# Kernel optimization log

Hardware: AMD Instinct MI355X
Metric: run time of the kernel (lower is better)

## Reference

```python
import jax, jax.numpy as jnp
import numpy as np

NHEAD = 4
DIM = 256

def rotate_half(x):
    # interleaved: out[..., ::2] = -x[..., 1::2]; out[..., 1::2] = x[..., ::2]
    xe = x[..., ::2]
    xo = x[..., 1::2]
    return jnp.stack([-xo, xe], axis=-1).reshape(x.shape)

def rope_2d(q, k, H, W):
    Dh = q.shape[-1]
    half = Dh // 2
    inv_freq = 1.0 / (10000.0 ** (jnp.arange(half, dtype=jnp.float32) / half))  # [half]
    yy, xx = jnp.meshgrid(jnp.arange(H, dtype=jnp.float32), jnp.arange(W, dtype=jnp.float32), indexing='ij')
    ang_y = yy.reshape(-1)[:, None] * inv_freq  # [N, half]
    ang_x = xx.reshape(-1)[:, None] * inv_freq  # [N, half]
    cy, sy = jnp.cos(ang_y), jnp.sin(ang_y)
    cx, sx = jnp.cos(ang_x), jnp.sin(ang_x)
    def rot(t):
        t1 = t[..., :half]          # y-rotated half
        t2 = t[..., half:2 * half]  # x-rotated half
        ty = t1 * cy + rotate_half(t1) * sy
        tx = t2 * cx + rotate_half(t2) * sx
        return jnp.concatenate([ty, tx, t[..., 2 * half:]], axis=-1)
    return rot(q), rot(k)

def layernorm(x, g, b, eps=1e-5):
    mu = jnp.mean(x, axis=-1, keepdims=True)
    var = jnp.var(x, axis=-1, keepdims=True)
    return (x - mu) / jnp.sqrt(var + eps) * g + b

def setup_inputs() -> dict:
    key = jax.random.key(0)
    ks = jax.random.split(key, 8)
    B, Hs, Ws, C = 4, 48, 48, DIM
    N = Hs * Ws
    s = 0.02
    return {
        'x': jax.random.normal(ks[0], (B, N, C), dtype=jnp.float32),
        'Wqkv': jax.random.normal(ks[1], (3 * C, C), dtype=jnp.float32) * s,
        'Wproj': jax.random.normal(ks[2], (C, C), dtype=jnp.float32) * s,
        'g1': jnp.ones((C,), jnp.float32), 'b1': jnp.zeros((C,), jnp.float32),
        'g2': jnp.ones((C,), jnp.float32), 'b2': jnp.zeros((C,), jnp.float32),
        'W1': jax.random.normal(ks[3], (4 * C, C), dtype=jnp.float32) * s,
        'bf1': jnp.zeros((4 * C,), jnp.float32),
        'W2': jax.random.normal(ks[4], (C, 4 * C), dtype=jnp.float32) * s,
        'bf2': jnp.zeros((C,), jnp.float32),
        'H': Hs, 'W': Ws,
    }

def reference(x, Wqkv, Wproj, g1, b1, g2, b2, W1, bf1, W2, bf2, H, W):
    B, N, C = x.shape
    dh = C // NHEAD
    qkv = (x @ Wqkv.T).reshape(B, N, 3, NHEAD, dh).transpose(2, 0, 3, 1, 4)  # [3,B,h,N,dh]
    q, k, v = qkv[0], qkv[1], qkv[2]
    q, k = rope_2d(q, k, H, W)
    scores = jnp.einsum('bhnd,bhmd->bhnm', q, k) / jnp.sqrt(jnp.float32(dh))
    attn = jax.nn.softmax(scores, axis=-1)  # drop_attn is identity (p=0)
    out = jnp.einsum('bhnm,bhmd->bhnd', attn, v).transpose(0, 2, 1, 3).reshape(B, N, C)
    x = x + out @ Wproj.T
    x = layernorm(x, g1, b1)
    h = jax.nn.gelu(x @ W1.T + bf1, approximate=False)
    x = x + h @ W2.T + bf2
    return layernorm(x, g2, b2)
```

## Files before the change

### kernel.cpp

```cpp
#include <hip/hip_runtime.h>
#include <hip/hip_bf16.h>
#include <math.h>

typedef __hip_bfloat16 bf16;
typedef __attribute__((ext_vector_type(8))) short short8;
typedef __attribute__((ext_vector_type(4))) short short4v;
typedef __attribute__((ext_vector_type(4))) float f32x4;
typedef __attribute__((ext_vector_type(4))) unsigned int u32x4;

#define NSEQ 2304
#define CDIM 256
#define NHD  4
#define DH   64

#if __has_builtin(__builtin_amdgcn_exp2f)
#define EXP2F __builtin_amdgcn_exp2f
#else
#define EXP2F exp2f
#endif

static __device__ __forceinline__ f32x4 mfma_bf16(short8 a, short8 b, f32x4 c) {
  return __builtin_amdgcn_mfma_f32_16x16x32_bf16(a, b, c, 0, 0, 0);
}
static __device__ __forceinline__ short8 ld8(const bf16* p) {
  return *reinterpret_cast<const short8*>(p);
}
static __device__ __forceinline__ short8 lds8(const bf16* p) {
  return *reinterpret_cast<const short8*>(p);
}
static __device__ __forceinline__ float b2f(short v) {
  unsigned int u = ((unsigned int)(unsigned short)v) << 16;
  return __uint_as_float(u);
}
static __device__ __forceinline__ short f2b(float f) {
  bf16 h = __float2bfloat16(f);
  return *reinterpret_cast<short*>(&h);
}
static __device__ __forceinline__ int swzb(int row, int off) {
  return (row << 7) + (off ^ ((row & 7) << 4));
}

__global__ __launch_bounds__(256) void detect_kernel(const void* __restrict__ xraw,
                                                     int* __restrict__ flag) {
  int t = threadIdx.x;
  const unsigned short* s = (const unsigned short*)xraw;
  int bad = 0;
#pragma unroll
  for (int i = 0; i < 8; ++i) {
    unsigned idx = (((unsigned)(t * 8 + i)) * 9173u) & ((1u << 20) - 1);
    unsigned short v = s[idx * 2];
    unsigned e = (v >> 7) & 0xFFu;
    if (e > 133u) bad++;
  }
  __shared__ int tot;
  if (t == 0) tot = 0;
  __syncthreads();
  atomicAdd(&tot, bad);
  __syncthreads();
  if (t == 0) flag[0] = (tot >= 16) ? 1 : 0;
}

__global__ __launch_bounds__(256) void cvt_all_kernel(const void* sx, const void* sqkv, const void* sproj,
                                                      const void* sw1, const void* sw2,
                                                      const void* g1, const void* b1, const void* g2,
                                                      const void* b2, const void* bias1, const void* bias2,
                                                      bf16* dx, bf16* dqkv, bf16* dproj,
                                                      bf16* dw1, bf16* dw2, bf16* dsm,
                                                      const int* __restrict__ flag) {
  int is32 = flag[0];
  int bid = blockIdx.x;
  const void* src; bf16* dst; int i4;
  if (bid < 2304)      { src = sx;    dst = dx;    i4 = bid * 256 + threadIdx.x; }
  else if (bid < 2496) { src = sqkv;  dst = dqkv;  i4 = (bid - 2304) * 256 + threadIdx.x; }
  else if (bid < 2560) { src = sproj; dst = dproj; i4 = (bid - 2496) * 256 + threadIdx.x; }
  else if (bid < 2816) { src = sw1;   dst = dw1;   i4 = (bid - 2560) * 256 + threadIdx.x; }
  else if (bid < 3072) { src = sw2;   dst = dw2;   i4 = (bid - 2816) * 256 + threadIdx.x; }
  else {
    const void* srcs[6] = {g1, b1, g2, b2, bias1, bias2};
    const int ns[6] = {256, 256, 256, 256, 1024, 256};
    const int off[6] = {0, 256, 512, 768, 1024, 2048};
    int t = threadIdx.x;
#pragma unroll
    for (int j = 0; j < 6; ++j)
      for (int i = t; i < ns[j]; i += 256) {
        if (is32) dsm[off[j] + i] = __float2bfloat16(((const float*)srcs[j])[i]);
        else      dsm[off[j] + i] = ((const bf16*)srcs[j])[i];
      }
    return;
  }
  if (is32) {
    float4 v = ((const float4*)src)[i4];
    short4v o;
    o[0] = f2b(v.x); o[1] = f2b(v.y); o[2] = f2b(v.z); o[3] = f2b(v.w);
    ((short4v*)dst)[i4] = o;
  } else {
    ((short4v*)dst)[i4] = ((const short4v*)src)[i4];
  }
}

__global__ __launch_bounds__(256, 1) void qkv_kernel(const bf16* __restrict__ X,
                                                     const bf16* __restrict__ Wqkv,
                                                     bf16* __restrict__ Q, bf16* __restrict__ K,
                                                     bf16* __restrict__ Vt,
                                                     const int* __restrict__ Wp) {
  int wave = threadIdx.x >> 6, lane = threadIdx.x & 63;
  int l15 = lane & 15, quad = lane >> 4;
  int m0 = (blockIdx.x * 4 + wave) * 64;
  int n0 = blockIdx.y * 64;
  const bf16* arow = X + (size_t)(m0 + l15) * CDIM + quad * 8;
  const bf16* brow = Wqkv + (size_t)(n0 + l15) * CDIM + quad * 8;
  f32x4 z = {0.f, 0.f, 0.f, 0.f};
  f32x4 acc[4][4];
#pragma unroll
  for (int j = 0; j < 4; ++j)
#pragma unroll
    for (int i = 0; i < 4; ++i) acc[j][i] = z;

  short8 a[4], b[4];
#pragma unroll
  for (int i = 0; i < 4; ++i) a[i] = ld8(arow + (size_t)i * 16 * CDIM);
#pragma unroll
  for (int j = 0; j < 4; ++j) b[j] = ld8(brow + (size_t)j * 16 * CDIM);
#pragma unroll
  for (int kk = 32; kk <= CDIM; kk += 32) {
    short8 an[4], bn[4];
    if (kk < CDIM) {
#pragma unroll
      for (int i = 0; i < 4; ++i) an[i] = ld8(arow + (size_t)i * 16 * CDIM + kk);
#pragma unroll
      for (int j = 0; j < 4; ++j) bn[j] = ld8(brow + (size_t)j * 16 * CDIM + kk);
    }
#pragma unroll
    for (int j = 0; j < 4; ++j)
#pragma unroll
      for (int i = 0; i < 4; ++i) acc[j][i] = mfma_bf16(b[j], a[i], acc[j][i]);
    if (kk < CDIM) {
#pragma unroll
      for (int i = 0; i < 4; ++i) a[i] = an[i];
#pragma unroll
      for (int j = 0; j < 4; ++j) b[j] = bn[j];
    }
  }

  int which = n0 >> 8, h = (n0 & 255) >> 6;
  if (which == 2) {
#pragma unroll
    for (int j = 0; j < 4; ++j) {
      int d0 = j * 16 + quad * 4;
#pragma unroll
      for (int i = 0; i < 4; ++i) {
        int gm = m0 + i * 16 + l15;
        int bb = gm / NSEQ, n = gm % NSEQ;
        int bh = bb * NHD + h;
#pragma unroll
        for (int r = 0; r < 4; ++r)
          Vt[((size_t)bh * DH + d0 + r) * NSEQ + n] = __float2bfloat16(acc[j][i][r]);
      }
    }
  } else {
    int Wv = Wp[0];
    if (Wv <= 0 || Wv > 65536) Wv = 48;
    bf16* dst = (which == 0) ? Q : K;
    const float cc = -0.28782313662425574f;
    const float EC1 = 0.7498942434f, EC2 = 0.5623413252f, EC3 = 0.4216965034f;
#pragma unroll
    for (int i = 0; i < 4; ++i) {
      int gm = m0 + i * 16 + l15;
      int bb = gm / NSEQ, n = gm % NSEQ;
      int bh = bb * NHD + h;
      int py = n / Wv, px = n - py * Wv;
#pragma unroll
      for (int j = 0; j < 4; ++j) {
        int d0 = j * 16 + quad * 4;
        float pos = (d0 & 32) ? (float)px : (float)py;
        int base = d0 & 31;
        float fb = __expf(cc * (float)base);
        float f0 = fb, f1 = fb * EC1, f2 = fb * EC2, f3 = fb * EC3;
        float s0, c0, s1, c1, s2, c2, s3, c3;
        __sincosf(pos * f0, &s0, &c0);
        __sincosf(pos * f1, &s1, &c1);
        __sincosf(pos * f2, &s2, &c2);
        __sincosf(pos * f3, &s3, &c3);
        float a0 = acc[j][i][0], a1 = acc[j][i][1], a2 = acc[j][i][2], a3 = acc[j][i][3];
        short4v ov;
        ov[0] = f2b(a0 * c0 - a1 * s0);
        ov[1] = f2b(a1 * c1 + a0 * s1);
        ov[2] = f2b(a2 * c2 - a3 * s2);
        ov[3] = f2b(a3 * c3 + a2 * s3);
        *reinterpret_cast<short4v*>(dst + ((size_t)bh * NSEQ + n) * DH + d0) = ov;
      }
    }
  }
}

__global__ __launch_bounds__(256, 4) void attn_kernel(const bf16* __restrict__ Q, const bf16* __restrict__ K,
                                                      const bf16* __restrict__ Vt, bf16* __restrict__ AO) {
  int bh = blockIdx.x, qt = blockIdx.y;
  int tid = threadIdx.x;
  int wave = tid >> 6, lane = tid & 63;
  int l15 = lane & 15, quad = lane >> 4;
  int qf = wave & 1;
  int ks = wave >> 1;
  int m0 = qt * 64 + qf * 32;
  const bf16* Qb = Q + (size_t)bh * NSEQ * DH;
  const bf16* Kb = K + (size_t)bh * NSEQ * DH;
  const bf16* Vb = Vt + (size_t)bh * DH * NSEQ;

  __shared__ __align__(16) char smem[32768];

  int r1 = tid >> 3, c1b = (tid & 7) * 16;
  int r1b = r1 + 32;

  const float QS = 0.18033688011112042f;
  short8 qa0 = ld8(Qb + (size_t)(m0 + l15) * DH + quad * 8);
  short8 qa1 = ld8(Qb + (size_t)(m0 + l15) * DH + 32 + quad * 8);
  short8 qb0 = ld8(Qb + (size_t)(m0 + 16 + l15) * DH + quad * 8);
  short8 qb1 = ld8(Qb + (size_t)(m0 + 16 + l15) * DH + 32 + quad * 8);
#pragma unroll
  for (int i = 0; i < 8; ++i) {
    qa0[i] = f2b(b2f(qa0[i]) * QS);
    qa1[i] = f2b(b2f(qa1[i]) * QS);
    qb0[i] = f2b(b2f(qb0[i]) * QS);
    qb1[i] = f2b(b2f(qb1[i]) * QS);
  }

  f32x4 z = {0.f, 0.f, 0.f, 0.f};
  f32x4 o[4] = {z, z, z, z};
  f32x4 o2[4] = {z, z, z, z};
  float l_run = 0.f, l_run2 = 0.f;

  *reinterpret_cast<short8*>(smem + swzb(r1, c1b))          = ld8(Kb + (size_t)r1 * DH + c1b / 2);
  *reinterpret_cast<short8*>(smem + swzb(r1b, c1b))         = ld8(Kb + (size_t)r1b * DH + c1b / 2);
  *reinterpret_cast<short8*>(smem + 16384 + swzb(r1, c1b))  = ld8(Vb + (size_t)r1 * NSEQ + c1b / 2);
  *reinterpret_cast<short8*>(smem + 16384 + swzb(r1b, c1b)) = ld8(Vb + (size_t)r1b * NSEQ + c1b / 2);
  __syncthreads();

  for (int it = 0; it < NSEQ / 64; ++it) {
    int cur = it & 1;
    bool more = (it + 1 < NSEQ / 64);

    short8 kpA, kpB, vpA, vpB;
    if (more) {
      int kn = (it + 1) * 64;
      kpA = ld8(Kb + (size_t)(kn + r1) * DH + c1b / 2);
      kpB = ld8(Kb + (size_t)(kn + r1b) * DH + c1b / 2);
      vpA = ld8(Vb + (size_t)r1 * NSEQ + kn + c1b / 2);
      vpB = ld8(Vb + (size_t)r1b * NSEQ + kn + c1b / 2);
    }

    const char* kb = smem + cur * 8192;
    const char* vb = smem + 16384 + cur * 8192;

    f32x4 s[2], s2[2];
#pragma unroll
    for (int kt = 0; kt < 2; ++kt) {
      int krow = ks * 32 + kt * 16 + l15;
      short8 kf0 = *reinterpret_cast<const short8*>(kb + swzb(krow, quad * 16));
      short8 kf1 = *reinterpret_cast<const short8*>(kb + swzb(krow, quad * 16 + 64));
      s[kt] = mfma_bf16(kf0, qa0, z);
      s[kt] = mfma_bf16(kf1, qa1, s[kt]);
      s2[kt] = mfma_bf16(kf0, qb0, z);
      s2[kt] = mfma_bf16(kf1, qb1, s2[kt]);
    }

    unsigned int A0, B0, A1, B1, C0, D0, C1, D1;
    {
      float p00 = EXP2F(s[0][0]), p01 = EXP2F(s[0][1]), p02 = EXP2F(s[0][2]), p03 = EXP2F(s[0][3]);
      float p10 = EXP2F(s[1][0]), p11 = EXP2F(s[1][1]), p12 = EXP2F(s[1][2]), p13 = EXP2F(s[1][3]);
      l_run += ((p00 + p01) + (p02 + p03)) + ((p10 + p11) + (p12 + p13));
      asm("v_cvt_pk_bf16_f32 %0, %1, %2" : "=v"(A0) : "v"(p00), "v"(p01));
      asm("v_cvt_pk_bf16_f32 %0, %1, %2" : "=v"(B0) : "v"(p02), "v"(p03));
      asm("v_cvt_pk_bf16_f32 %0, %1, %2" : "=v"(A1) : "v"(p10), "v"(p11));
      asm("v_cvt_pk_bf16_f32 %0, %1, %2" : "=v"(B1) : "v"(p12), "v"(p13));
      float q00 = EXP2F(s2[0][0]), q01 = EXP2F(s2[0][1]), q02 = EXP2F(s2[0][2]), q03 = EXP2F(s2[0][3]);
      float q10 = EXP2F(s2[1][0]), q11 = EXP2F(s2[1][1]), q12 = EXP2F(s2[1][2]), q13 = EXP2F(s2[1][3]);
      l_run2 += ((q00 + q01) + (q02 + q03)) + ((q10 + q11) + (q12 + q13));
      asm("v_cvt_pk_bf16_f32 %0, %1, %2" : "=v"(C0) : "v"(q00), "v"(q01));
      asm("v_cvt_pk_bf16_f32 %0, %1, %2" : "=v"(D0) : "v"(q02), "v"(q03));
      asm("v_cvt_pk_bf16_f32 %0, %1, %2" : "=v"(C1) : "v"(q10), "v"(q11));
      asm("v_cvt_pk_bf16_f32 %0, %1, %2" : "=v"(D1) : "v"(q12), "v"(q13));
    }
    asm("v_permlane32_swap_b32 %0, %1" : "+v"(A0), "+v"(A1));
    asm("v_permlane16_swap_b32 %0, %1" : "+v"(A0), "+v"(A1));
    asm("v_permlane32_swap_b32 %0, %1" : "+v"(B0), "+v"(B1));
    asm("v_permlane16_swap_b32 %0, %1" : "+v"(B0), "+v"(B1));
    asm("v_permlane32_swap_b32 %0, %1" : "+v"(C0), "+v"(C1));
    asm("v_permlane16_swap_b32 %0, %1" : "+v"(C0), "+v"(C1));
    asm("v_permlane32_swap_b32 %0, %1" : "+v"(D0), "+v"(D1));
    asm("v_permlane16_swap_b32 %0, %1" : "+v"(D0), "+v"(D1));

    u32x4 wA; wA[0] = A0; wA[1] = B0; wA[2] = A1; wA[3] = B1;
    u32x4 wB; wB[0] = C0; wB[1] = D0; wB[2] = C1; wB[3] = D1;
    short8 pfA = *reinterpret_cast<short8*>(&wA);
    short8 pfB = *reinterpret_cast<short8*>(&wB);

#pragma unroll
    for (int t = 0; t < 4; ++t) {
      short8 vf = *reinterpret_cast<const short8*>(vb + swzb(t * 16 + l15, ks * 64 + quad * 16));
      o[t] = mfma_bf16(vf, pfA, o[t]);
      o2[t] = mfma_bf16(vf, pfB, o2[t]);
    }

    if (more) {
      char* kn_ = smem + (1 - cur) * 8192;
      char* vn_ = smem + 16384 + (1 - cur) * 8192;
      *reinterpret_cast<short8*>(kn_ + swzb(r1, c1b))  = kpA;
      *reinterpret_cast<short8*>(kn_ + swzb(r1b, c1b)) = kpB;
      *reinterpret_cast<short8*>(vn_ + swzb(r1, c1b))  = vpA;
      *reinterpret_cast<short8*>(vn_ + swzb(r1b, c1b)) = vpB;
    }
    __syncthreads();
  }

  float* scr = (float*)smem;
  int slot = qf * 64 + lane;
  if (ks == 1) {
    float* p = scr + slot * 36;
#pragma unroll
    for (int t = 0; t < 4; ++t) {
      *reinterpret_cast<f32x4*>(p + t * 4) = o[t];
      *reinterpret_cast<f32x4*>(p + 16 + t * 4) = o2[t];
    }
    p[32] = l_run;
    p[33] = l_run2;
  }
  __syncthreads();
  if (ks == 0) {
    float* p = scr + slot * 36;
#pragma unroll
    for (int t = 0; t < 4; ++t) {
      f32x4 pa = *reinterpret_cast<f32x4*>(p + t * 4);
      f32x4 pb2 = *reinterpret_cast<f32x4*>(p + 16 + t * 4);
#pragma unroll
      for (int r = 0; r < 4; ++r) {
        o[t][r] += pa[r];
        o2[t][r] += pb2[r];
      }
    }
    l_run += p[32];
    l_run2 += p[33];

    l_run += __shfl_xor(l_run, 16);
    l_run += __shfl_xor(l_run, 32);
    l_run2 += __shfl_xor(l_run2, 16);
    l_run2 += __shfl_xor(l_run2, 32);
    float inv = 1.f / l_run;
    float inv2 = 1.f / l_run2;
    int b = bh >> 2, h = bh & 3;
    bf16* orow = AO + ((size_t)b * NSEQ + (m0 + l15)) * CDIM + h * DH;
    bf16* orow2 = AO + ((size_t)b * NSEQ + (m0 + 16 + l15)) * CDIM + h * DH;
#pragma unroll
    for (int t = 0; t < 4; ++t) {
      short4v ov, ov2;
#pragma unroll
      for (int r = 0; r < 4; ++r) {
        ov[r] = f2b(o[t][r] * inv);
        ov2[r] = f2b(o2[t][r] * inv2);
      }
      *reinterpret_cast<short4v*>(orow + t * 16 + quad * 4) = ov;
      *reinterpret_cast<short4v*>(orow2 + t * 16 + quad * 4) = ov2;
    }
  }
}

template <int KD, int EPI, int TI>
__global__ __launch_bounds__(256) void gemm128(const bf16* __restrict__ A, const bf16* __restrict__ Wm,
                                               const bf16* __restrict__ bias, const bf16* __restrict__ res,
                                               bf16* __restrict__ outp, int NC) {
  constexpr int KS = KD / 32;
  constexpr int AR = TI * 32;
  int tid = threadIdx.x;
  int wave = tid >> 6, lane = tid & 63;
  int l15 = lane & 15, quad = lane >> 4;
  int wm = (wave >> 1) * (TI * 16);
  int wn = (wave & 1) * 64;
  int m0 = blockIdx.x * AR;
  int n0 = blockIdx.y * 128;

  __shared__ __align__(16) bf16 abuf[2][AR * 40];
  __shared__ __align__(16) bf16 bbuf[2][128 * 40];

  int sr = tid >> 2, sc = (tid & 3) * 8;

  const bf16* ag[TI / 2];
#pragma unroll
  for (int u = 0; u < TI / 2; ++u) ag[u] = A + (size_t)(m0 + sr + u * 64) * KD + sc;
  const bf16* bg0 = Wm + (size_t)(n0 + sr) * KD + sc;
  const bf16* bg1 = Wm + (size_t)(n0 + 64 + sr) * KD + sc;

  f32x4 z = {0.f, 0.f, 0.f, 0.f};
  f32x4 acc[4][TI];
#pragma unroll
  for (int j = 0; j < 4; ++j)
#pragma unroll
    for (int i = 0; i < TI; ++i) acc[j][i] = z;

#pragma unroll
  for (int u = 0; u < TI / 2; ++u)
    *reinterpret_cast<short8*>(abuf[0] + (sr + u * 64) * 40 + sc) = ld8(ag[u]);
  *reinterpret_cast<short8*>(bbuf[0] + sr * 40 + sc) = ld8(bg0);
  *reinterpret_cast<short8*>(bbuf[0] + (64 + sr) * 40 + sc) = ld8(bg1);
  __syncthreads();

  for (int s = 0; s < KS; ++s) {
    int cur = s & 1;
    bool more = (s + 1 < KS);
    short8 anx[TI / 2], bnx0, bnx1;
    if (more) {
#pragma unroll
      for (int u = 0; u < TI / 2; ++u) anx[u] = ld8(ag[u] + (s + 1) * 32);
      bnx0 = ld8(bg0 + (s + 1) * 32);
      bnx1 = ld8(bg1 + (s + 1) * 32);
    }
    short8 af[TI], bf_[4];
#pragma unroll
    for (int i = 0; i < TI; ++i)
      af[i] = lds8(abuf[cur] + (size_t)(wm + i * 16 + l15) * 40 + quad * 8);
#pragma unroll
    for (int j = 0; j < 4; ++j)
      bf_[j] = lds8(bbuf[cur] + (size_t)(wn + j * 16 + l15) * 40 + quad * 8);
#pragma unroll
    for (int j = 0; j < 4; ++j)
#pragma unroll
      for (int i = 0; i < TI; ++i)
        acc[j][i] = mfma_bf16(bf_[j], af[i], acc[j][i]);
    if (more) {
#pragma unroll
      for (int u = 0; u < TI / 2; ++u)
        *reinterpret_cast<short8*>(abuf[1 - cur] + (sr + u * 64) * 40 + sc) = anx[u];
      *reinterpret_cast<short8*>(bbuf[1 - cur] + sr * 40 + sc) = bnx0;
      *reinterpret_cast<short8*>(bbuf[1 - cur] + (64 + sr) * 40 + sc) = bnx1;
    }
    __syncthreads();
  }

#pragma unroll
  for (int j = 0; j < 4; ++j) {
    int col0 = n0 + wn + j * 16 + quad * 4;
    float bb4[4];
    if (EPI != 0) {
      short4v bl = *reinterpret_cast<const short4v*>(bias + col0);
#pragma unroll
      for (int r = 0; r < 4; ++r) bb4[r] = b2f(bl[r]);
    }
#pragma unroll
    for (int i = 0; i < TI; ++i) {
      size_t idx = (size_t)(m0 + wm + i * 16 + l15) * NC + col0;
      short4v ov;
      if (EPI == 0) {
        short4v rl = *reinterpret_cast<const short4v*>(res + idx);
#pragma unroll
        for (int r = 0; r < 4; ++r) ov[r] = f2b(acc[j][i][r] + b2f(rl[r]));
      } else if (EPI == 1) {
#pragma unroll
        for (int r = 0; r < 4; ++r) {
          float hv = acc[j][i][r] + bb4[r];
          ov[r] = f2b(0.5f * hv * (1.f + erff(hv * 0.70710678118f)));
        }
      } else {
        short4v rl = *reinterpret_cast<const short4v*>(res + idx);
#pragma unroll
        for (int r = 0; r < 4; ++r) ov[r] = f2b(acc[j][i][r] + bb4[r] + b2f(rl[r]));
      }
      *reinterpret_cast<short4v*>(outp + idx) = ov;
    }
  }
}

template <int KD, int HASBIAS, int FINAL>
__global__ __launch_bounds__(256) void gemm_ln(const bf16* __restrict__ A, const bf16* __restrict__ Wm,
                                               const bf16* __restrict__ bias, const bf16* __restrict__ res,
                                               const bf16* __restrict__ g, const bf16* __restrict__ bv,
                                               void* __restrict__ outp, const int* __restrict__ flag) {
  constexpr int KS = KD / 32;
  int tid = threadIdx.x;
  int wave = tid >> 6, lane = tid & 63;
  int l15 = lane & 15, quad = lane >> 4;
  int wn = wave * 64;
  int m0 = blockIdx.x * 32;
  int is32 = FINAL ? flag[0] : 0;

  __shared__ __align__(16) bf16 abuf[2][32 * 40];
  __shared__ __align__(16) bf16 bbuf[2][256 * 40];
  __shared__ float red[4][32][2];

  int sr = tid >> 2, sc = (tid & 3) * 8;
  bool doA = tid < 128;
  int ra = tid >> 2, ca = (tid & 3) * 8;

  const bf16* ag = A + (size_t)(m0 + ra) * KD + ca;
  const bf16* bg[4];
#pragma unroll
  for (int u = 0; u < 4; ++u) bg[u] = Wm + (size_t)(sr + u * 64) * KD + sc;

  f32x4 z = {0.f, 0.f, 0.f, 0.f};
  f32x4 acc[4][2];
#pragma unroll
  for (int j = 0; j < 4; ++j)
#pragma unroll
    for (int i = 0; i < 2; ++i) acc[j][i] = z;

  if (doA) *reinterpret_cast<short8*>(abuf[0] + ra * 40 + ca) = ld8(ag);
#pragma unroll
  for (int u = 0; u < 4; ++u)
    *reinterpret_cast<short8*>(bbuf[0] + (sr + u * 64) * 40 + sc) = ld8(bg[u]);
  __syncthreads();

  for (int s = 0; s < KS; ++s) {
    int cur = s & 1;
    bool more = (s + 1 < KS);
    short8 anx, bnx[4];
    if (more) {
      if (doA) anx = ld8(ag + (s + 1) * 32);
#pragma unroll
      for (int u = 0; u < 4; ++u) bnx[u] = ld8(bg[u] + (s + 1) * 32);
    }
    short8 af[2], bf_[4];
#pragma unroll
    for (int i = 0; i < 2; ++i)
      af[i] = lds8(abuf[cur] + (size_t)(i * 16 + l15) * 40 + quad * 8);
#pragma unroll
    for (int j = 0; j < 4; ++j)
      bf_[j] = lds8(bbuf[cur] + (size_t)(wn + j * 16 + l15) * 40 + quad * 8);
#pragma unroll
    for (int j = 0; j < 4; ++j)
#pragma unroll
      for (int i = 0; i < 2; ++i)
        acc[j][i] = mfma_bf16(bf_[j], af[i], acc[j][i]);
    if (more) {
      if (doA) *reinterpret_cast<short8*>(abuf[1 - cur] + ra * 40 + ca) = anx;
#pragma unroll
      for (int u = 0; u < 4; ++u)
        *reinterpret_cast<short8*>(bbuf[1 - cur] + (sr + u * 64) * 40 + sc) = bnx[u];
    }
    __syncthreads();
  }

  float bb[4][4];
  if (HASBIAS) {
#pragma unroll
    for (int j = 0; j < 4; ++j) {
      short4v bl = *reinterpret_cast<const short4v*>(bias + wn + j * 16 + quad * 4);
#pragma unroll
      for (int r = 0; r < 4; ++r) bb[j][r] = b2f(bl[r]);
    }
  }
  float vals[2][4][4];
  float s0 = 0.f, q0 = 0.f, s1 = 0.f, q1 = 0.f;
#pragma unroll
  for (int i = 0; i < 2; ++i) {
    int row = m0 + i * 16 + l15;
#pragma unroll
    for (int j = 0; j < 4; ++j) {
      int col0 = wn + j * 16 + quad * 4;
      short4v rl = *reinterpret_cast<const short4v*>(res + (size_t)row * CDIM + col0);
#pragma unroll
      for (int r = 0; r < 4; ++r) {
        float v = acc[j][i][r] + (HASBIAS ? bb[j][r] : 0.f) + b2f(rl[r]);
        vals[i][j][r] = v;
        if (i == 0) { s0 += v; q0 += v * v; }
        else        { s1 += v; q1 += v * v; }
      }
    }
  }
  s0 += __shfl_xor(s0, 16); s0 += __shfl_xor(s0, 32);
  q0 += __shfl_xor(q0, 16); q0 += __shfl_xor(q0, 32);
  s1 += __shfl_xor(s1, 16); s1 += __shfl_xor(s1, 32);
  q1 += __shfl_xor(q1, 16); q1 += __shfl_xor(q1, 32);
  if (quad == 0) {
    red[wave][l15][0] = s0;      red[wave][l15][1] = q0;
    red[wave][16 + l15][0] = s1; red[wave][16 + l15][1] = q1;
  }
  __syncthreads();

#pragma unroll
  for (int i = 0; i < 2; ++i) {
    int rl_ = i * 16 + l15;
    float S = 0.f, Q = 0.f;
#pragma unroll
    for (int w = 0; w < 4; ++w) { S += red[w][rl_][0]; Q += red[w][rl_][1]; }
    float mu = S * (1.f / CDIM);
    float var = Q * (1.f / CDIM) - mu * mu;
    float rstd = rsqrtf(var + 1e-5f);
    int row = m0 + i * 16 + l15;
#pragma unroll
    for (int j = 0; j < 4; ++j) {
      int col0 = wn + j * 16 + quad * 4;
      short4v gl = *reinterpret_cast<const short4v*>(g + col0);
      short4v bl2 = *reinterpret_cast<const short4v*>(bv + col0);
      size_t idx = (size_t)row * CDIM + col0;
      if (FINAL && is32) {
        float4 ov;
        ov.x = (vals[i][j][0] - mu) * rstd * b2f(gl[0]) + b2f(bl2[0]);
        ov.y = (vals[i][j][1] - mu) * rstd * b2f(gl[1]) + b2f(bl2[1]);
        ov.z = (vals[i][j][2] - mu) * rstd * b2f(gl[2]) + b2f(bl2[2]);
        ov.w = (vals[i][j][3] - mu) * rstd * b2f(gl[3]) + b2f(bl2[3]);
        *reinterpret_cast<float4*>((float*)outp + idx) = ov;
      } else {
        short4v ov;
#pragma unroll
        for (int r = 0; r < 4; ++r)
          ov[r] = f2b((vals[i][j][r] - mu) * rstd * b2f(gl[r]) + b2f(bl2[r]));
        *reinterpret_cast<short4v*>((bf16*)outp + idx) = ov;
      }
    }
  }
}

extern "C" void kernel_launch(void* const* d_in, const int* in_sizes, int n_in,
                              void* d_out, int out_size, void* d_ws, size_t ws_size,
                              hipStream_t stream) {
  const int* Wp = (const int*)d_in[12];

  char* ws = (char*)d_ws;
  const size_t SZ = 4718592;
  bf16* Qc  = (bf16*)(ws + 0 * SZ);
  bf16* Kc  = (bf16*)(ws + 1 * SZ);
  bf16* Vt  = (bf16*)(ws + 2 * SZ);
  bf16* AO  = (bf16*)(ws + 3 * SZ);
  bf16* F   = (bf16*)(ws + 4 * SZ);
  bf16* xc  = (bf16*)(ws + 6 * SZ);
  bf16* G   = (bf16*)(ws + 0);
  bf16* Wqkvc  = (bf16*)(ws + 7 * SZ);
  bf16* Wprojc = (bf16*)(ws + 7 * SZ + 393216);
  bf16* W1c    = (bf16*)(ws + 7 * SZ + 524288);
  bf16* W2c    = (bf16*)(ws + 7 * SZ + 1048576);
  bf16* smallc = (bf16*)(ws + 7 * SZ + 1572864);
  bf16* g1c  = smallc + 0;
  bf16* b1c  = smallc + 256;
  bf16* g2c  = smallc + 512;
  bf16* b2c  = smallc + 768;
  bf16* bf1c = smallc + 1024;
  bf16* bf2c = smallc + 2048;
  int*  flagp = (int*)(ws + 7 * SZ + 1581568);

  detect_kernel<<<1, 256, 0, stream>>>(d_in[0], flagp);
  cvt_all_kernel<<<3073, 256, 0, stream>>>(d_in[0], d_in[1], d_in[2], d_in[7], d_in[9],
                                           d_in[3], d_in[4], d_in[5], d_in[6], d_in[8], d_in[10],
                                           xc, Wqkvc, Wprojc, W1c, W2c, smallc, flagp);

  qkv_kernel<<<dim3(36, 12), 256, 0, stream>>>(xc, Wqkvc, Qc, Kc, Vt, Wp);
  attn_kernel<<<dim3(16, 36), 256, 0, stream>>>(Qc, Kc, Vt, AO);
  gemm_ln<256, 0, 0><<<288, 256, 0, stream>>>(AO, Wprojc, nullptr, xc, g1c, b1c, F, flagp);
  gemm128<256, 1, 4><<<dim3(72, 8), 256, 0, stream>>>(F, W1c, bf1c, nullptr, G, 1024);
  gemm_ln<1024, 1, 1><<<288, 256, 0, stream>>>(G, W2c, bf2c, F, g2c, b2c, d_out, flagp);
}
```

Baseline: 206.9 us.

## Replace shared-memory FC1 GEMM with register-only direct-load MFMA kernel

The FC1 GEMM (M=9216, N=1024, K=256) with fused bias and GELU moves from a 128x128 LDS double-buffered tiled kernel to one where each wave computes a 64x64 tile on its own. Operands are loaded straight from global memory into registers with one-step prefetch. This removes LDS traffic and block-wide barriers. In exchange, waves in a block no longer share A or B tiles, so global and L2 read traffic rises, and the loads are strided row reads rather than coalesced tiles.

```diff
diff --git a/kernel.cpp b/kernel.cpp
--- a/kernel.cpp
+++ b/kernel.cpp
@@ -193,6 +193,70 @@
   }
 }
 
+__global__ __launch_bounds__(256, 1) void fc1_kernel(const bf16* __restrict__ A,
+                                                     const bf16* __restrict__ Wm,
+                                                     const bf16* __restrict__ bias,
+                                                     bf16* __restrict__ outp) {
+  int wave = threadIdx.x >> 6, lane = threadIdx.x & 63;
+  int l15 = lane & 15, quad = lane >> 4;
+  int m0 = (blockIdx.x * 4 + wave) * 64;
+  int n0 = blockIdx.y * 64;
+  const bf16* arow = A + (size_t)(m0 + l15) * CDIM + quad * 8;
+  const bf16* brow = Wm + (size_t)(n0 + l15) * CDIM + quad * 8;
+  f32x4 z = {0.f, 0.f, 0.f, 0.f};
+  f32x4 acc[4][4];
+#pragma unroll
+  for (int j = 0; j < 4; ++j)
+#pragma unroll
+    for (int i = 0; i < 4; ++i) acc[j][i] = z;
+
+  short8 a[4], b[4];
+#pragma unroll
+  for (int i = 0; i < 4; ++i) a[i] = ld8(arow + (size_t)i * 16 * CDIM);
+#pragma unroll
+  for (int j = 0; j < 4; ++j) b[j] = ld8(brow + (size_t)j * 16 * CDIM);
+#pragma unroll
+  for (int kk = 32; kk <= CDIM; kk += 32) {
+    short8 an[4], bn[4];
+    if (kk < CDIM) {
+#pragma unroll
+      for (int i = 0; i < 4; ++i) an[i] = ld8(arow + (size_t)i * 16 * CDIM + kk);
+#pragma unroll
+      for (int j = 0; j < 4; ++j) bn[j] = ld8(brow + (size_t)j * 16 * CDIM + kk);
+    }
+#pragma unroll
+    for (int j = 0; j < 4; ++j)
+#pragma unroll
+      for (int i = 0; i < 4; ++i) acc[j][i] = mfma_bf16(b[j], a[i], acc[j][i]);
+    if (kk < CDIM) {
+#pragma unroll
+      for (int i = 0; i < 4; ++i) a[i] = an[i];
+#pragma unroll
+      for (int j = 0; j < 4; ++j) b[j] = bn[j];
+    }
+  }
+
+#pragma unroll
+  for (int j = 0; j < 4; ++j) {
+    int col0 = n0 + j * 16 + quad * 4;
+    short4v bl = *reinterpret_cast<const short4v*>(bias + col0);
+    float bb4[4];
+#pragma unroll
+    for (int r = 0; r < 4; ++r) bb4[r] = b2f(bl[r]);
+#pragma unroll
+    for (int i = 0; i < 4; ++i) {
+      int row = m0 + i * 16 + l15;
+      short4v ov;
+#pragma unroll
+      for (int r = 0; r < 4; ++r) {
+        float hv = acc[j][i][r] + bb4[r];
+        ov[r] = f2b(0.5f * hv * (1.f + erff(hv * 0.70710678118f)));
+      }
+      *reinterpret_cast<short4v*>(outp + (size_t)row * 1024 + col0) = ov;
+    }
+  }
+}
+
 __global__ __launch_bounds__(256, 4) void attn_kernel(const bf16* __restrict__ Q, const bf16* __restrict__ K,
                                                       const bf16* __restrict__ Vt, bf16* __restrict__ AO) {
   int bh = blockIdx.x, qt = blockIdx.y;
@@ -359,110 +423,6 @@
       }
       *reinterpret_cast<short4v*>(orow + t * 16 + quad * 4) = ov;
       *reinterpret_cast<short4v*>(orow2 + t * 16 + quad * 4) = ov2;
-    }
-  }
-}
-
-template <int KD, int EPI, int TI>
-__global__ __launch_bounds__(256) void gemm128(const bf16* __restrict__ A, const bf16* __restrict__ Wm,
-                                               const bf16* __restrict__ bias, const bf16* __restrict__ res,
-                                               bf16* __restrict__ outp, int NC) {
-  constexpr int KS = KD / 32;
-  constexpr int AR = TI * 32;
-  int tid = threadIdx.x;
-  int wave = tid >> 6, lane = tid & 63;
-  int l15 = lane & 15, quad = lane >> 4;
-  int wm = (wave >> 1) * (TI * 16);
-  int wn = (wave & 1) * 64;
-  int m0 = blockIdx.x * AR;
-  int n0 = blockIdx.y * 128;
-
-  __shared__ __align__(16) bf16 abuf[2][AR * 40];
-  __shared__ __align__(16) bf16 bbuf[2][128 * 40];
-
-  int sr = tid >> 2, sc = (tid & 3) * 8;
-
-  const bf16* ag[TI / 2];
-#pragma unroll
-  for (int u = 0; u < TI / 2; ++u) ag[u] = A + (size_t)(m0 + sr + u * 64) * KD + sc;
-  const bf16* bg0 = Wm + (size_t)(n0 + sr) * KD + sc;
-  const bf16* bg1 = Wm + (size_t)(n0 + 64 + sr) * KD + sc;
-
-  f32x4 z = {0.f, 0.f, 0.f, 0.f};
-  f32x4 acc[4][TI];
-#pragma unroll
-  for (int j = 0; j < 4; ++j)
-#pragma unroll
-    for (int i = 0; i < TI; ++i) acc[j][i] = z;
-
-#pragma unroll
-  for (int u = 0; u < TI / 2; ++u)
-    *reinterpret_cast<short8*>(abuf[0] + (sr + u * 64) * 40 + sc) = ld8(ag[u]);
-  *reinterpret_cast<short8*>(bbuf[0] + sr * 40 + sc) = ld8(bg0);
-  *reinterpret_cast<short8*>(bbuf[0] + (64 + sr) * 40 + sc) = ld8(bg1);
-  __syncthreads();
-
-  for (int s = 0; s < KS; ++s) {
-    int cur = s & 1;
-    bool more = (s + 1 < KS);
-    short8 anx[TI / 2], bnx0, bnx1;
-    if (more) {
-#pragma unroll
-      for (int u = 0; u < TI / 2; ++u) anx[u] = ld8(ag[u] + (s + 1) * 32);
-      bnx0 = ld8(bg0 + (s + 1) * 32);
-      bnx1 = ld8(bg1 + (s + 1) * 32);
-    }
-    short8 af[TI], bf_[4];
-#pragma unroll
-    for (int i = 0; i < TI; ++i)
-      af[i] = lds8(abuf[cur] + (size_t)(wm + i * 16 + l15) * 40 + quad * 8);
-#pragma unroll
-    for (int j = 0; j < 4; ++j)
-      bf_[j] = lds8(bbuf[cur] + (size_t)(wn + j * 16 + l15) * 40 + quad * 8);
-#pragma unroll
-    for (int j = 0; j < 4; ++j)
-#pragma unroll
-      for (int i = 0; i < TI; ++i)
-        acc[j][i] = mfma_bf16(bf_[j], af[i], acc[j][i]);
-    if (more) {
-#pragma unroll
-      for (int u = 0; u < TI / 2; ++u)
-        *reinterpret_cast<short8*>(abuf[1 - cur] + (sr + u * 64) * 40 + sc) = anx[u];
-      *reinterpret_cast<short8*>(bbuf[1 - cur] + sr * 40 + sc) = bnx0;
-      *reinterpret_cast<short8*>(bbuf[1 - cur] + (64 + sr) * 40 + sc) = bnx1;
-    }
-    __syncthreads();
-  }
-
-#pragma unroll
-  for (int j = 0; j < 4; ++j) {
-    int col0 = n0 + wn + j * 16 + quad * 4;
-    float bb4[4];
-    if (EPI != 0) {
-      short4v bl = *reinterpret_cast<const short4v*>(bias + col0);
-#pragma unroll
-      for (int r = 0; r < 4; ++r) bb4[r] = b2f(bl[r]);
-    }
-#pragma unroll
-    for (int i = 0; i < TI; ++i) {
-      size_t idx = (size_t)(m0 + wm + i * 16 + l15) * NC + col0;
-      short4v ov;
-      if (EPI == 0) {
-        short4v rl = *reinterpret_cast<const short4v*>(res + idx);
-#pragma unroll
-        for (int r = 0; r < 4; ++r) ov[r] = f2b(acc[j][i][r] + b2f(rl[r]));
-      } else if (EPI == 1) {
-#pragma unroll
-        for (int r = 0; r < 4; ++r) {
-          float hv = acc[j][i][r] + bb4[r];
-          ov[r] = f2b(0.5f * hv * (1.f + erff(hv * 0.70710678118f)));
-        }
-      } else {
-        short4v rl = *reinterpret_cast<const short4v*>(res + idx);
-#pragma unroll
-        for (int r = 0; r < 4; ++r) ov[r] = f2b(acc[j][i][r] + bb4[r] + b2f(rl[r]));
-      }
-      *reinterpret_cast<short4v*>(outp + idx) = ov;
     }
   }
 }
@@ -642,6 +602,6 @@
   qkv_kernel<<<dim3(36, 12), 256, 0, stream>>>(xc, Wqkvc, Qc, Kc, Vt, Wp);
   attn_kernel<<<dim3(16, 36), 256, 0, stream>>>(Qc, Kc, Vt, AO);
   gemm_ln<256, 0, 0><<<288, 256, 0, stream>>>(AO, Wprojc, nullptr, xc, g1c, b1c, F, flagp);
-  gemm128<256, 1, 4><<<dim3(72, 8), 256, 0, stream>>>(F, W1c, bf1c, nullptr, G, 1024);
+  fc1_kernel<<<dim3(36, 16), 256, 0, stream>>>(F, W1c, bf1c, G);
   gemm_ln<1024, 1, 1><<<288, 256, 0, stream>>>(G, W2c, bf2c, F, g2c, b2c, d_out, flagp);
 }
```

Result: slower. 220.3 us (+6.5%).
